# Kernel tuning notes

Measured on AMD Instinct MI355X. Metric: run time of the kernel, lower is better.

Reference implementation:

```python
import jax, jax.numpy as jnp
import numpy as np

B, S, D = 4, 2048, 1024
KEY_DIM, VALUE_DIM = 1024, 1024
BETA = 1.0 / np.sqrt(D)  # beta defaults to 1/sqrt(input dim), per build()


def setup_inputs() -> dict:
    key = jax.random.key(0)
    ks = jax.random.split(key, 9)
    inv = 1.0 / np.sqrt(D)
    return {
        "query": jax.random.normal(ks[0], (B, S, D), dtype=jnp.float32),
        "key": jax.random.normal(ks[1], (B, S, D), dtype=jnp.float32),
        "value": jax.random.normal(ks[2], (B, S, D), dtype=jnp.float32),
        "Wq": jax.random.normal(ks[3], (D, KEY_DIM), dtype=jnp.float32) * inv,
        "bq": jnp.zeros((KEY_DIM,), dtype=jnp.float32),
        "Wk": jax.random.normal(ks[4], (D, KEY_DIM), dtype=jnp.float32) * inv,
        "bk": jnp.zeros((KEY_DIM,), dtype=jnp.float32),
        "Wv": jax.random.normal(ks[5], (D, VALUE_DIM), dtype=jnp.float32) * inv,
        "bv": jnp.zeros((VALUE_DIM,), dtype=jnp.float32),
    }


def reference(query, key, value, Wq, bq, Wk, bk, Wv, bv):
    # Dense projections
    q = query @ Wq + bq          # [B, S, key_dim]
    k = key @ Wk + bk            # [B, S, key_dim]
    v = value @ Wv + bv          # [B, S, value_dim]
    # Scaled dot-product attention (beta applied AFTER matmul, as in source)
    scores = jnp.einsum("bik,bjk->bij", q, k)  # [B, S, S]
    A = jax.nn.softmax(BETA * scores, axis=-1)
    return jnp.einsum("bij,bjk->bik", A, v)    # [B, S, value_dim]
```

## Files before the change

### kernel.cpp

```cpp
#include <hip/hip_runtime.h>


typedef __bf16 bf16x8 __attribute__((ext_vector_type(8)));
typedef float f32x4 __attribute__((ext_vector_type(4)));

#define MIB ((size_t)1 << 20)

__device__ __forceinline__ unsigned short f2b(float f) {
  unsigned int u = __float_as_uint(f);
  return (unsigned short)((u + 0x7FFFu + ((u >> 16) & 1u)) >> 16);
}

__device__ __forceinline__ void async16(const void* g, void* l) {
  __builtin_amdgcn_global_load_lds(
      (const __attribute__((address_space(1))) unsigned int*)g,
      (__attribute__((address_space(3))) unsigned int*)l, 16, 0, 0);
}

__device__ __forceinline__ unsigned ldsoff(const unsigned short* p) {
  return (unsigned)(size_t)(const __attribute__((address_space(3))) unsigned short*)p;
}

__device__ __forceinline__ bf16x8 ds_read16(unsigned off) {
  bf16x8 r;
  asm volatile("ds_read_b128 %0, %1" : "=v"(r) : "v"(off));
  return r;
}

template <int TN>
__device__ __forceinline__ void stage_tile(
    const unsigned short* __restrict__ A, const unsigned short* __restrict__ Bt,
    unsigned short* dst, int K, int kb, int tid) {
#pragma unroll
  for (int i = 0; i < 4; ++i) {
    const int e = i * 256 + tid;
    const int r = e >> 3;
    const int cg = (e & 7) ^ (r & 7);
    async16(A + (size_t)r * K + kb + cg * 8, dst + e * 8);
  }
#pragma unroll
  for (int i = 0; i < TN / 32; ++i) {
    const int e = i * 256 + tid;
    const int r = e >> 3;
    const int cg = (e & 7) ^ (r & 7);
    async16(Bt + (size_t)r * K + kb + cg * 8, dst + 128 * 64 + e * 8);
  }
}

template <int TN, bool SWAP>
__device__ __forceinline__ void gemm_loop(
    const unsigned short* __restrict__ A, const unsigned short* __restrict__ Bt,
    unsigned short* lds, int K, int m0, int n0, f32x4 (&acc)[4][TN / 32]) {
  constexpr int NI = TN / 32;
  constexpr unsigned BUFB = (128 + TN) * 64 * 2;
  const int tid = threadIdx.x;
  const int lane = tid & 63;
  const int wave = tid >> 6;
  const int wm = (wave >> 1) * 64;
  const int wn = (wave & 1) * (TN / 2);
  const int fr = lane & 15;
  const int q = lane >> 4;
  const int NT = K >> 6;

  const unsigned short* Ab = A + (size_t)m0 * K;
  const unsigned short* Bb = Bt + (size_t)n0 * K;
  const unsigned LB = ldsoff(lds);

  unsigned oa[4][2], ob[NI][2];
#pragma unroll
  for (int mi = 0; mi < 4; ++mi) {
    const int R = wm + mi * 16 + fr;
#pragma unroll
    for (int ks = 0; ks < 2; ++ks) {
      const int kc = ks * 4 + q;
      oa[mi][ks] = (unsigned)((R * 64 + ((kc ^ (R & 7)) << 3)) * 2);
    }
  }
#pragma unroll
  for (int ni = 0; ni < NI; ++ni) {
    const int R = wn + ni * 16 + fr;
#pragma unroll
    for (int ks = 0; ks < 2; ++ks) {
      const int kc = ks * 4 + q;
      ob[ni][ks] =
          (unsigned)(128 * 64 * 2 + (R * 64 + ((kc ^ (R & 7)) << 3)) * 2);
    }
  }

  stage_tile<TN>(Ab, Bb, lds, K, 0, tid);
  __syncthreads();

  for (int t = 0; t < NT; ++t) {
    const unsigned boff = LB + (unsigned)(t & 1) * BUFB;
    if (t + 1 < NT)
      stage_tile<TN>(Ab, Bb, lds + ((t + 1) & 1) * (BUFB / 2), K,
                     (t + 1) << 6, tid);

    bf16x8 av[2][4], bv[2][NI];
#pragma unroll
    for (int ks = 0; ks < 2; ++ks)
#pragma unroll
      for (int mi = 0; mi < 4; ++mi) av[ks][mi] = ds_read16(boff + oa[mi][ks]);
#pragma unroll
    for (int ks = 0; ks < 2; ++ks)
#pragma unroll
      for (int ni = 0; ni < NI; ++ni) bv[ks][ni] = ds_read16(boff + ob[ni][ks]);

    asm volatile("s_waitcnt lgkmcnt(0)");
    __builtin_amdgcn_sched_barrier(0);

#pragma unroll
    for (int ks = 0; ks < 2; ++ks)
#pragma unroll
      for (int mi = 0; mi < 4; ++mi)
#pragma unroll
        for (int ni = 0; ni < NI; ++ni)
          acc[mi][ni] = SWAP ? __builtin_amdgcn_mfma_f32_16x16x32_bf16(
                                   bv[ks][ni], av[ks][mi], acc[mi][ni], 0, 0, 0)
                             : __builtin_amdgcn_mfma_f32_16x16x32_bf16(
                                   av[ks][mi], bv[ks][ni], acc[mi][ni], 0, 0, 0);

    __syncthreads();
  }
}

struct ProjArgs {
  const unsigned short* A[3];
  const unsigned short* Bt[3];
  unsigned short* C[3];
  const float* bias[3];
};

__global__ __launch_bounds__(256) void proj_qk(ProjArgs p) {
  __shared__ __align__(16) unsigned short lds[2 * 256 * 64];
  const int z = blockIdx.z;
  const int m0 = blockIdx.y * 128;
  const int n0 = blockIdx.x * 128;

  f32x4 acc[4][4] = {};
  gemm_loop<128, true>(p.A[z], p.Bt[z], lds, 1024, m0, n0, acc);

  const int lane = threadIdx.x & 63;
  const int wave = threadIdx.x >> 6;
  const int wm = (wave >> 1) * 64;
  const int wn = (wave & 1) * 64;
  const int fr = lane & 15;
  const int q4 = (lane >> 4) * 4;
  const float* bias = p.bias[z];
  unsigned short* C = p.C[z];

#pragma unroll
  for (int mi = 0; mi < 4; ++mi) {
    const int m = m0 + wm + mi * 16 + fr;
#pragma unroll
    for (int ni = 0; ni < 4; ++ni) {
      const int nb = n0 + wn + ni * 16 + q4;
      const float4 bb = *(const float4*)&bias[nb];
      ushort4 o = make_ushort4(
          f2b(acc[mi][ni][0] + bb.x), f2b(acc[mi][ni][1] + bb.y),
          f2b(acc[mi][ni][2] + bb.z), f2b(acc[mi][ni][3] + bb.w));
      *(ushort4*)&C[(size_t)m * 1024 + nb] = o;
    }
  }
}

__global__ __launch_bounds__(256) void proj_v(ProjArgs p) {
  __shared__ __align__(16) unsigned short lds[2 * 256 * 64];
  const int m0 = blockIdx.y * 128;
  const int n0 = blockIdx.x * 128;

  f32x4 acc[4][4] = {};
  gemm_loop<128, false>(p.A[2], p.Bt[2], lds, 1024, m0, n0, acc);

  const int lane = threadIdx.x & 63;
  const int wave = threadIdx.x >> 6;
  const int wm = (wave >> 1) * 64;
  const int wn = (wave & 1) * 64;
  const int fr = lane & 15;
  const int q4 = (lane >> 4) * 4;
  const float* bias = p.bias[2];

  unsigned short* C = p.C[2] + (size_t)(m0 >> 11) * (2048 * 1024);
#pragma unroll
  for (int mi = 0; mi < 4; ++mi) {
#pragma unroll
    for (int ni = 0; ni < 4; ++ni) {
      const int col = n0 + wn + ni * 16 + fr;
      const float bb = bias[col];
      const int rowb = (m0 + wm + mi * 16 + q4) & 2047;
      ushort4 o =
          make_ushort4(f2b(acc[mi][ni][0] + bb), f2b(acc[mi][ni][1] + bb),
                       f2b(acc[mi][ni][2] + bb), f2b(acc[mi][ni][3] + bb));
      *(ushort4*)&C[(size_t)col * 2048 + rowb] = o;
    }
  }
}

__global__ __launch_bounds__(256) void gemm_f32(
    const unsigned short* __restrict__ A, const unsigned short* __restrict__ Bt,
    float* __restrict__ C, int K, int ldc, long long sA, long long sB,
    long long sC) {
  __shared__ __align__(16) unsigned short lds[2 * 256 * 64];
  const int bz = blockIdx.z;
  A += (long long)bz * sA;
  Bt += (long long)bz * sB;
  C += (long long)bz * sC;
  const int m0 = blockIdx.y * 128;
  const int n0 = blockIdx.x * 128;

  f32x4 acc[4][4] = {};
  gemm_loop<128, true>(A, Bt, lds, K, m0, n0, acc);

  const int lane = threadIdx.x & 63;
  const int wave = threadIdx.x >> 6;
  const int wm = (wave >> 1) * 64;
  const int wn = (wave & 1) * 64;
  const int fr = lane & 15;
  const int q4 = (lane >> 4) * 4;
#pragma unroll
  for (int mi = 0; mi < 4; ++mi) {
    const int m = m0 + wm + mi * 16 + fr;
#pragma unroll
    for (int ni = 0; ni < 4; ++ni) {
      const int nb = n0 + wn + ni * 16 + q4;
      *(f32x4*)&C[(size_t)m * ldc + nb] = acc[mi][ni];
    }
  }
}

__global__ __launch_bounds__(256) void cast3(
    const float4* __restrict__ a, const float4* __restrict__ b,
    const float4* __restrict__ c, ushort4* __restrict__ oa,
    ushort4* __restrict__ ob, ushort4* __restrict__ oc, int n4) {
  const int i = blockIdx.x * 256 + threadIdx.x;
  if (i >= n4) return;
  const float4* src = (blockIdx.y == 0) ? a : (blockIdx.y == 1) ? b : c;
  ushort4* dst = (blockIdx.y == 0) ? oa : (blockIdx.y == 1) ? ob : oc;
  float4 v = src[i];
  dst[i] = make_ushort4(f2b(v.x), f2b(v.y), f2b(v.z), f2b(v.w));
}

__global__ __launch_bounds__(256) void transpose3(
    const float* __restrict__ w0, const float* __restrict__ w1,
    const float* __restrict__ w2, unsigned short* __restrict__ t0,
    unsigned short* __restrict__ t1, unsigned short* __restrict__ t2) {
  __shared__ float t[32][33];
  const int K = 1024, N = 1024;
  const float* W = (blockIdx.z == 0) ? w0 : (blockIdx.z == 1) ? w1 : w2;
  unsigned short* WT = (blockIdx.z == 0) ? t0 : (blockIdx.z == 1) ? t1 : t2;
  const int n0 = blockIdx.x * 32, k0 = blockIdx.y * 32;
  const int tx = threadIdx.x, ty = threadIdx.y;
#pragma unroll
  for (int i = 0; i < 32; i += 8)
    t[ty + i][tx] = W[(size_t)(k0 + ty + i) * N + (n0 + tx)];
  __syncthreads();
#pragma unroll
  for (int i = 0; i < 32; i += 8)
    WT[(size_t)(n0 + ty + i) * K + (k0 + tx)] = f2b(t[tx][ty + i]);
}

__global__ __launch_bounds__(256) void softmax_rows(const float* __restrict__ S,
                                                    unsigned short* __restrict__ P) {
  const int cols = 2048;
  const size_t row = blockIdx.x;
  const float4* srow = (const float4*)(S + row * cols);
  const int tid = threadIdx.x;
  const int lane = tid & 63;
  const int wave = tid >> 6;

  float4 a = srow[tid];
  float4 b = srow[tid + 256];

  float mx = fmaxf(fmaxf(fmaxf(a.x, a.y), fmaxf(a.z, a.w)),
                   fmaxf(fmaxf(b.x, b.y), fmaxf(b.z, b.w)));
#pragma unroll
  for (int o = 1; o < 64; o <<= 1) mx = fmaxf(mx, __shfl_xor(mx, o));

  __shared__ float red[8];
  if (lane == 0) red[wave] = mx;
  __syncthreads();
  mx = fmaxf(fmaxf(red[0], red[1]), fmaxf(red[2], red[3]));

  const float c = 0.03125f * 1.4426950408889634f;
  float4 pa, pb;
  pa.x = exp2f((a.x - mx) * c); pa.y = exp2f((a.y - mx) * c);
  pa.z = exp2f((a.z - mx) * c); pa.w = exp2f((a.w - mx) * c);
  pb.x = exp2f((b.x - mx) * c); pb.y = exp2f((b.y - mx) * c);
  pb.z = exp2f((b.z - mx) * c); pb.w = exp2f((b.w - mx) * c);

  float sum = pa.x + pa.y + pa.z + pa.w + pb.x + pb.y + pb.z + pb.w;
#pragma unroll
  for (int o = 1; o < 64; o <<= 1) sum += __shfl_xor(sum, o);
  if (lane == 0) red[4 + wave] = sum;
  __syncthreads();
  sum = red[4] + red[5] + red[6] + red[7];

  const float inv = 1.0f / sum;
  ushort4* prow = (ushort4*)(P + row * cols);
  prow[tid] = make_ushort4(f2b(pa.x * inv), f2b(pa.y * inv), f2b(pa.z * inv),
                           f2b(pa.w * inv));
  prow[tid + 256] = make_ushort4(f2b(pb.x * inv), f2b(pb.y * inv),
                                 f2b(pb.z * inv), f2b(pb.w * inv));
}

extern "C" void kernel_launch(void* const* d_in, const int* in_sizes, int n_in,
                              void* d_out, int out_size, void* d_ws, size_t ws_size,
                              hipStream_t stream) {
  const float* query = (const float*)d_in[0];
  const float* key_ = (const float*)d_in[1];
  const float* value = (const float*)d_in[2];
  const float* Wq = (const float*)d_in[3];
  const float* bq = (const float*)d_in[4];
  const float* Wk = (const float*)d_in[5];
  const float* bk = (const float*)d_in[6];
  const float* Wv = (const float*)d_in[7];
  const float* bv = (const float*)d_in[8];
  float* out = (float*)d_out;

  char* ws = (char*)d_ws;
  unsigned short* WqT = (unsigned short*)ws;
  unsigned short* WkT = WqT + (size_t)1024 * 1024;
  unsigned short* WvT = WkT + (size_t)1024 * 1024;
  unsigned short* Xq = (unsigned short*)(ws + 6 * MIB);
  unsigned short* Xk = Xq + (size_t)8192 * 1024;
  unsigned short* Xv = Xk + (size_t)8192 * 1024;
  unsigned short* qb = (unsigned short*)(ws + 54 * MIB);
  unsigned short* kb = (unsigned short*)(ws + 70 * MIB);
  unsigned short* vT = (unsigned short*)(ws + 86 * MIB);
  float* sc = (float*)(ws + 102 * MIB);
  unsigned short* P = (unsigned short*)(ws + 6 * MIB);

  const int n4 = (4 * 2048 * 1024) / 4;
  cast3<<<dim3(n4 / 256, 3), 256, 0, stream>>>(
      (const float4*)query, (const float4*)key_, (const float4*)value,
      (ushort4*)Xq, (ushort4*)Xk, (ushort4*)Xv, n4);

  transpose3<<<dim3(32, 32, 3), dim3(32, 8), 0, stream>>>(Wq, Wk, Wv, WqT, WkT,
                                                          WvT);

  ProjArgs pa;
  pa.A[0] = Xq;  pa.A[1] = Xk;  pa.A[2] = Xv;
  pa.Bt[0] = WqT; pa.Bt[1] = WkT; pa.Bt[2] = WvT;
  pa.C[0] = qb;  pa.C[1] = kb;  pa.C[2] = vT;
  pa.bias[0] = bq; pa.bias[1] = bk; pa.bias[2] = bv;

  proj_qk<<<dim3(8, 64, 2), 256, 0, stream>>>(pa);
  proj_v<<<dim3(8, 64, 1), 256, 0, stream>>>(pa);

  gemm_f32<<<dim3(16, 16, 4), 256, 0, stream>>>(
      qb, kb, sc, 1024, 2048, 2048LL * 1024, 2048LL * 1024, 2048LL * 2048);

  softmax_rows<<<8192, 256, 0, stream>>>(sc, P);

  gemm_f32<<<dim3(8, 16, 4), 256, 0, stream>>>(
      P, vT, out, 2048, 1024, 2048LL * 2048, 1024LL * 2048, 2048LL * 1024);
}
```

Baseline: 337.4 us.

## Fuse fp32-to-bf16 input cast into projection GEMM staging

Drops the separate cast kernel for query/key/value. The projection GEMMs now stage fp32 activation tiles into LDS directly with an XOR swizzle and convert them to bf16 in registers before the MFMAs. This removes a full write and re-read of three bf16 activation copies and one launch. In exchange each tile moves twice the A-side bytes through LDS and adds conversion work in the inner loop, with single buffering and a full wait on the LDS reads.

```diff
diff --git a/kernel.cpp b/kernel.cpp
--- a/kernel.cpp
+++ b/kernel.cpp
@@ -17,14 +17,120 @@
       (__attribute__((address_space(3))) unsigned int*)l, 16, 0, 0);
 }
 
-__device__ __forceinline__ unsigned ldsoff(const unsigned short* p) {
-  return (unsigned)(size_t)(const __attribute__((address_space(3))) unsigned short*)p;
+__device__ __forceinline__ unsigned ldsoff(const void* p) {
+  return (unsigned)(size_t)(const __attribute__((address_space(3))) char*)p;
 }
 
 __device__ __forceinline__ bf16x8 ds_read16(unsigned off) {
   bf16x8 r;
   asm volatile("ds_read_b128 %0, %1" : "=v"(r) : "v"(off));
   return r;
+}
+__device__ __forceinline__ f32x4 ds_read16f(unsigned off) {
+  f32x4 r;
+  asm volatile("ds_read_b128 %0, %1" : "=v"(r) : "v"(off));
+  return r;
+}
+
+__device__ __forceinline__ bf16x8 cvt8(f32x4 lo, f32x4 hi) {
+  bf16x8 r;
+  r[0] = (__bf16)lo[0]; r[1] = (__bf16)lo[1];
+  r[2] = (__bf16)lo[2]; r[3] = (__bf16)lo[3];
+  r[4] = (__bf16)hi[0]; r[5] = (__bf16)hi[1];
+  r[6] = (__bf16)hi[2]; r[7] = (__bf16)hi[3];
+  return r;
+}
+
+__device__ __forceinline__ void stage_tile_f32(
+    const float* __restrict__ A, const unsigned short* __restrict__ Bt,
+    char* dst, int K, int kb, int tid) {
+#pragma unroll
+  for (int i = 0; i < 8; ++i) {
+    const int e = i * 256 + tid;
+    const int r = e >> 4;
+    const int cg = (e & 15) ^ ((r & 7) << 1);
+    async16(A + (size_t)r * K + kb + cg * 4, dst + e * 16);
+  }
+#pragma unroll
+  for (int i = 0; i < 4; ++i) {
+    const int e = i * 256 + tid;
+    const int r = e >> 3;
+    const int cg = (e & 7) ^ (r & 7);
+    async16(Bt + (size_t)r * K + kb + cg * 8, dst + 32768 + e * 16);
+  }
+}
+
+template <bool SWAP>
+__device__ __forceinline__ void gemm_loop_proj(
+    const float* __restrict__ A, const unsigned short* __restrict__ Bt,
+    char* lds, int K, int m0, int n0, f32x4 (&acc)[4][4]) {
+  const int tid = threadIdx.x;
+  const int lane = tid & 63;
+  const int wave = tid >> 6;
+  const int wm = (wave >> 1) * 64;
+  const int wn = (wave & 1) * 64;
+  const int fr = lane & 15;
+  const int q = lane >> 4;
+  const int NT = K >> 6;
+
+  const float* Ab = A + (size_t)m0 * K;
+  const unsigned short* Bb = Bt + (size_t)n0 * K;
+  const unsigned LB = ldsoff(lds);
+
+  unsigned oa[2][4], ob[2][4];
+#pragma unroll
+  for (int mi = 0; mi < 4; ++mi) {
+    const int R = wm + mi * 16 + fr;
+#pragma unroll
+    for (int ks = 0; ks < 2; ++ks) {
+      const int kc = ks * 4 + q;
+      oa[ks][mi] = (unsigned)(R * 256 + (((2 * kc) ^ ((R & 7) << 1)) << 4));
+    }
+  }
+#pragma unroll
+  for (int ni = 0; ni < 4; ++ni) {
+    const int R = wn + ni * 16 + fr;
+#pragma unroll
+    for (int ks = 0; ks < 2; ++ks) {
+      const int kc = ks * 4 + q;
+      ob[ks][ni] = (unsigned)(32768 + R * 128 + ((kc ^ (R & 7)) << 4));
+    }
+  }
+
+  for (int t = 0; t < NT; ++t) {
+    stage_tile_f32(Ab, Bb, lds, K, t << 6, tid);
+    __syncthreads();
+
+#pragma unroll
+    for (int ks = 0; ks < 2; ++ks) {
+      f32x4 alo[4], ahi[4];
+      bf16x8 bv[4];
+#pragma unroll
+      for (int mi = 0; mi < 4; ++mi) {
+        alo[mi] = ds_read16f(LB + oa[ks][mi]);
+        ahi[mi] = ds_read16f(LB + oa[ks][mi] + 16);
+      }
+#pragma unroll
+      for (int ni = 0; ni < 4; ++ni) bv[ni] = ds_read16(LB + ob[ks][ni]);
+
+      asm volatile("s_waitcnt lgkmcnt(0)");
+      __builtin_amdgcn_sched_barrier(0);
+
+      bf16x8 av[4];
+#pragma unroll
+      for (int mi = 0; mi < 4; ++mi) av[mi] = cvt8(alo[mi], ahi[mi]);
+
+#pragma unroll
+      for (int mi = 0; mi < 4; ++mi)
+#pragma unroll
+        for (int ni = 0; ni < 4; ++ni)
+          acc[mi][ni] = SWAP ? __builtin_amdgcn_mfma_f32_16x16x32_bf16(
+                                   bv[ni], av[mi], acc[mi][ni], 0, 0, 0)
+                             : __builtin_amdgcn_mfma_f32_16x16x32_bf16(
+                                   av[mi], bv[ni], acc[mi][ni], 0, 0, 0);
+    }
+    __syncthreads();
+  }
 }
 
 template <int TN>
@@ -125,20 +231,20 @@
 }
 
 struct ProjArgs {
-  const unsigned short* A[3];
+  const float* A[3];
   const unsigned short* Bt[3];
   unsigned short* C[3];
   const float* bias[3];
 };
 
 __global__ __launch_bounds__(256) void proj_qk(ProjArgs p) {
-  __shared__ __align__(16) unsigned short lds[2 * 256 * 64];
+  __shared__ __align__(16) char lds[49152];
   const int z = blockIdx.z;
   const int m0 = blockIdx.y * 128;
   const int n0 = blockIdx.x * 128;
 
   f32x4 acc[4][4] = {};
-  gemm_loop<128, true>(p.A[z], p.Bt[z], lds, 1024, m0, n0, acc);
+  gemm_loop_proj<true>(p.A[z], p.Bt[z], lds, 1024, m0, n0, acc);
 
   const int lane = threadIdx.x & 63;
   const int wave = threadIdx.x >> 6;
@@ -165,12 +271,12 @@
 }
 
 __global__ __launch_bounds__(256) void proj_v(ProjArgs p) {
-  __shared__ __align__(16) unsigned short lds[2 * 256 * 64];
+  __shared__ __align__(16) char lds[49152];
   const int m0 = blockIdx.y * 128;
   const int n0 = blockIdx.x * 128;
 
   f32x4 acc[4][4] = {};
-  gemm_loop<128, false>(p.A[2], p.Bt[2], lds, 1024, m0, n0, acc);
+  gemm_loop_proj<false>(p.A[2], p.Bt[2], lds, 1024, m0, n0, acc);
 
   const int lane = threadIdx.x & 63;
   const int wave = threadIdx.x >> 6;
@@ -226,18 +332,6 @@
       *(f32x4*)&C[(size_t)m * ldc + nb] = acc[mi][ni];
     }
   }
-}
-
-__global__ __launch_bounds__(256) void cast3(
-    const float4* __restrict__ a, const float4* __restrict__ b,
-    const float4* __restrict__ c, ushort4* __restrict__ oa,
-    ushort4* __restrict__ ob, ushort4* __restrict__ oc, int n4) {
-  const int i = blockIdx.x * 256 + threadIdx.x;
-  if (i >= n4) return;
-  const float4* src = (blockIdx.y == 0) ? a : (blockIdx.y == 1) ? b : c;
-  ushort4* dst = (blockIdx.y == 0) ? oa : (blockIdx.y == 1) ? ob : oc;
-  float4 v = src[i];
-  dst[i] = make_ushort4(f2b(v.x), f2b(v.y), f2b(v.z), f2b(v.w));
 }
 
 __global__ __launch_bounds__(256) void transpose3(
@@ -321,25 +415,17 @@
   unsigned short* WqT = (unsigned short*)ws;
   unsigned short* WkT = WqT + (size_t)1024 * 1024;
   unsigned short* WvT = WkT + (size_t)1024 * 1024;
-  unsigned short* Xq = (unsigned short*)(ws + 6 * MIB);
-  unsigned short* Xk = Xq + (size_t)8192 * 1024;
-  unsigned short* Xv = Xk + (size_t)8192 * 1024;
   unsigned short* qb = (unsigned short*)(ws + 54 * MIB);
   unsigned short* kb = (unsigned short*)(ws + 70 * MIB);
   unsigned short* vT = (unsigned short*)(ws + 86 * MIB);
   float* sc = (float*)(ws + 102 * MIB);
   unsigned short* P = (unsigned short*)(ws + 6 * MIB);
 
-  const int n4 = (4 * 2048 * 1024) / 4;
-  cast3<<<dim3(n4 / 256, 3), 256, 0, stream>>>(
-      (const float4*)query, (const float4*)key_, (const float4*)value,
-      (ushort4*)Xq, (ushort4*)Xk, (ushort4*)Xv, n4);
-
   transpose3<<<dim3(32, 32, 3), dim3(32, 8), 0, stream>>>(Wq, Wk, Wv, WqT, WkT,
                                                           WvT);
 
   ProjArgs pa;
-  pa.A[0] = Xq;  pa.A[1] = Xk;  pa.A[2] = Xv;
+  pa.A[0] = query;  pa.A[1] = key_;  pa.A[2] = value;
   pa.Bt[0] = WqT; pa.Bt[1] = WkT; pa.Bt[2] = WvT;
   pa.C[0] = qb;  pa.C[1] = kb;  pa.C[2] = vT;
   pa.bias[0] = bq; pa.bias[1] = bk; pa.bias[2] = bv;
```

After: 362.4 us. +7.4%, slower.
